# Kernel optimization log

Hardware: AMD Instinct MI355X
Metric: run time of the kernel (lower is better)

The kernel has to match this reference:

```python
import jax, jax.numpy as jnp
import numpy as np

HEADS = 8
DIM_HEAD = 64
DIM = 512
EPS = 1e-5


def setup_inputs() -> dict:
    key = jax.random.key(0)
    ks = jax.random.split(key, 4)
    b, n = 4, 2048
    inner = HEADS * DIM_HEAD
    x = jax.random.normal(ks[0], (b, n, DIM), dtype=jnp.float32)
    pose_bias = jax.random.normal(ks[1], (b, n), dtype=jnp.float32)
    ln_gamma = jnp.ones((DIM,), dtype=jnp.float32)
    ln_beta = jnp.zeros((DIM,), dtype=jnp.float32)
    w_qkv = jax.random.normal(ks[2], (DIM, 3 * inner), dtype=jnp.float32) * (DIM ** -0.5)
    w_out = jax.random.normal(ks[3], (inner, DIM), dtype=jnp.float32) * (inner ** -0.5)
    beta = jnp.float32(0.5)
    return {"x": x, "pose_bias": pose_bias, "ln_gamma": ln_gamma,
            "ln_beta": ln_beta, "w_qkv": w_qkv, "w_out": w_out, "beta": beta}


def reference(x, pose_bias, ln_gamma, ln_beta, w_qkv, w_out, beta):
    b, n, d = x.shape
    h, dh = HEADS, DIM_HEAD
    scale = dh ** -0.5
    # LayerNorm (biased variance, eps=1e-5, affine)
    mu = jnp.mean(x, axis=-1, keepdims=True)
    var = jnp.mean(jnp.square(x - mu), axis=-1, keepdims=True)
    xn = (x - mu) * jax.lax.rsqrt(var + EPS) * ln_gamma + ln_beta
    # fused QKV projection (no bias)
    qkv = xn @ w_qkv                                  # [b, n, 3*h*dh]
    q, k, v = jnp.split(qkv, 3, axis=-1)
    def to_heads(t):
        return t.reshape(b, n, h, dh).transpose(0, 2, 1, 3)  # [b, h, n, dh]
    q, k, v = to_heads(q), to_heads(k), to_heads(v)
    dots = jnp.einsum('bhnd,bhmd->bhnm', q, k) * scale  # [b, h, n, n]
    # additive pose bias: beta * (bias_i + bias_j), broadcast over heads
    pose_attn = beta * (pose_bias[:, None, :, None] + pose_bias[:, None, None, :])
    dots = dots + pose_attn
    attn = jax.nn.softmax(dots, axis=-1)
    out = jnp.einsum('bhnm,bhmd->bhnd', attn, v)       # [b, h, n, dh]
    out = out.transpose(0, 2, 1, 3).reshape(b, n, h * dh)
    return out @ w_out
```

## Files before the change

kernel.cpp:

```cpp
#include <hip/hip_runtime.h>

#define NH    8
#define DH    64
#define DIMD  512
#define NCTX  2048
#define NB    4
#define NROWS (NB * NCTX)
#define QKVN  (3 * DIMD)

typedef __attribute__((ext_vector_type(8))) short bf16x8;
typedef __attribute__((ext_vector_type(4))) float f32x4;

#define INV_LN2 1.44269504f
#define SCLOG   (0.125f * INV_LN2)

__device__ __forceinline__ unsigned short f2bits(float f) {
  unsigned u = __float_as_uint(f);
  u += 0x7fffu + ((u >> 16) & 1u);
  return (unsigned short)(u >> 16);
}
__device__ __forceinline__ float bits2f(unsigned short u) {
  return __uint_as_float(((unsigned)u) << 16);
}

__global__ __launch_bounds__(256) void ln_kernel(
    const float* __restrict__ x,
    const float* __restrict__ gamma,
    const float* __restrict__ beta,
    unsigned short* __restrict__ xn) {
  const int wid  = threadIdx.x >> 6;
  const int lane = threadIdx.x & 63;
  const int row  = blockIdx.x * 4 + wid;
  const float* xr = x + (size_t)row * DIMD + lane * 8;
  float v[8];
  const float4 a = *reinterpret_cast<const float4*>(xr);
  const float4 b = *reinterpret_cast<const float4*>(xr + 4);
  v[0] = a.x; v[1] = a.y; v[2] = a.z; v[3] = a.w;
  v[4] = b.x; v[5] = b.y; v[6] = b.z; v[7] = b.w;
  float s = 0.f;
#pragma unroll
  for (int i = 0; i < 8; ++i) s += v[i];
#pragma unroll
  for (int off = 32; off; off >>= 1) s += __shfl_down(s, off);
  s = __shfl(s, 0);
  const float mu = s * (1.f / DIMD);
  float ss = 0.f;
#pragma unroll
  for (int i = 0; i < 8; ++i) { float d = v[i] - mu; ss += d * d; }
#pragma unroll
  for (int off = 32; off; off >>= 1) ss += __shfl_down(ss, off);
  ss = __shfl(ss, 0);
  const float inv = rsqrtf(ss * (1.f / DIMD) + 1e-5f);
  const float4 g0 = *reinterpret_cast<const float4*>(gamma + lane * 8);
  const float4 g1 = *reinterpret_cast<const float4*>(gamma + lane * 8 + 4);
  const float4 b0 = *reinterpret_cast<const float4*>(beta + lane * 8);
  const float4 b1 = *reinterpret_cast<const float4*>(beta + lane * 8 + 4);
  float g[8] = {g0.x, g0.y, g0.z, g0.w, g1.x, g1.y, g1.z, g1.w};
  float be[8] = {b0.x, b0.y, b0.z, b0.w, b1.x, b1.y, b1.z, b1.w};
  bf16x8 o;
#pragma unroll
  for (int i = 0; i < 8; ++i)
    o[i] = (short)f2bits((v[i] - mu) * inv * g[i] + be[i]);
  *reinterpret_cast<bf16x8*>(xn + (size_t)row * DIMD + lane * 8) = o;
}

__global__ __launch_bounds__(256) void tconv_kernel(
    const float* __restrict__ in0, unsigned short* __restrict__ out0,
    const float* __restrict__ in1, unsigned short* __restrict__ out1) {
  const int z = blockIdx.z;
  const int C = z ? DIMD : QKVN;
  if (z && blockIdx.x >= DIMD / 64) return;
  const float* in = z ? in1 : in0;
  unsigned short* out = z ? out1 : out0;
  __shared__ float T[64][65];
  const int r0 = blockIdx.y * 64, c0 = blockIdx.x * 64;
  const int ty = threadIdx.x >> 4, tx = threadIdx.x & 15;
#pragma unroll
  for (int i = 0; i < 4; ++i) {
    const int r = ty + i * 16;
    const float4 v = *reinterpret_cast<const float4*>(
        in + (size_t)(r0 + r) * C + c0 + tx * 4);
    T[r][tx * 4 + 0] = v.x; T[r][tx * 4 + 1] = v.y;
    T[r][tx * 4 + 2] = v.z; T[r][tx * 4 + 3] = v.w;
  }
  __syncthreads();
#pragma unroll
  for (int i = 0; i < 4; ++i) {
    const int c = ty + i * 16;
    ushort4 o;
    o.x = f2bits(T[tx * 4 + 0][c]); o.y = f2bits(T[tx * 4 + 1][c]);
    o.z = f2bits(T[tx * 4 + 2][c]); o.w = f2bits(T[tx * 4 + 3][c]);
    *reinterpret_cast<ushort4*>(out + (size_t)(c0 + c) * DIMD + r0 + tx * 4) = o;
  }
}

__global__ __launch_bounds__(256) void vtrans_kernel(
    const unsigned short* __restrict__ qkv,
    const float* __restrict__ pb,
    const float* __restrict__ betap,
    unsigned short* __restrict__ cexp,
    unsigned short* __restrict__ vt) {
  __shared__ unsigned short T[64][68];
  const int jt = blockIdx.x, hi = blockIdx.y, bi = blockIdx.z;
  const int ty = threadIdx.x >> 4, tx = threadIdx.x & 15;
  const int j0 = jt * 64;
#pragma unroll
  for (int i = 0; i < 4; ++i) {
    const int j = ty + i * 16;
    const ushort4 v = *reinterpret_cast<const ushort4*>(
        qkv + (size_t)(bi * NCTX + j0 + j) * QKVN + 2 * DIMD + hi * DH + tx * 4);
    T[j][tx * 4 + 0] = v.x; T[j][tx * 4 + 1] = v.y;
    T[j][tx * 4 + 2] = v.z; T[j][tx * 4 + 3] = v.w;
  }
  const float bl2 = betap[0] * INV_LN2;
  const float4 pv = *reinterpret_cast<const float4*>(pb + bi * NCTX + j0 + tx * 4);
  ushort4 cb;
  cb.x = f2bits(exp2f(bl2 * pv.x)); cb.y = f2bits(exp2f(bl2 * pv.y));
  cb.z = f2bits(exp2f(bl2 * pv.z)); cb.w = f2bits(exp2f(bl2 * pv.w));
  if (hi == 0 && ty == 0)
    *reinterpret_cast<ushort4*>(cexp + bi * NCTX + j0 + tx * 4) = cb;
  const float c0 = bits2f(cb.x), c1 = bits2f(cb.y), c2 = bits2f(cb.z), c3 = bits2f(cb.w);
  __syncthreads();
#pragma unroll
  for (int i = 0; i < 4; ++i) {
    const int d = ty + i * 16;
    ushort4 o;
    o.x = f2bits(bits2f(T[tx * 4 + 0][d]) * c0);
    o.y = f2bits(bits2f(T[tx * 4 + 1][d]) * c1);
    o.z = f2bits(bits2f(T[tx * 4 + 2][d]) * c2);
    o.w = f2bits(bits2f(T[tx * 4 + 3][d]) * c3);
    *reinterpret_cast<ushort4*>(
        vt + ((size_t)(bi * NH + hi) * DH + d) * NCTX + j0 + tx * 4) = o;
  }
}

__device__ __forceinline__ void storeC(float* C, size_t idx, float v) { C[idx] = v; }
__device__ __forceinline__ void storeC(unsigned short* C, size_t idx, float v) { C[idx] = f2bits(v); }

template <typename CT, bool QS>
__global__ __launch_bounds__(256) void mgemm_kernel(
    const unsigned short* __restrict__ A, const unsigned short* __restrict__ Bt,
    CT* __restrict__ C, int M, int N, int K) {
  __shared__ __align__(16) unsigned short As[128][72];
  __shared__ __align__(16) unsigned short Bs[128][72];
  const int tid  = threadIdx.x;
  const int wave = tid >> 6, lane = tid & 63;
  const int quad = lane >> 4, l16 = lane & 15;
  const int wr = wave >> 1, wc = wave & 1;
  const int tm0 = blockIdx.y * 128, tn0 = blockIdx.x * 128;
  const int srow = tid >> 3;
  const int schunk = (tid & 7) * 8;
  f32x4 acc[4][4];
#pragma unroll
  for (int i = 0; i < 4; ++i)
#pragma unroll
    for (int j = 0; j < 4; ++j) acc[i][j] = (f32x4){0.f, 0.f, 0.f, 0.f};

  bf16x8 ra[4], rb[4];
#pragma unroll
  for (int p = 0; p < 4; ++p) {
    const int r = srow + p * 32;
    ra[p] = *reinterpret_cast<const bf16x8*>(A + (size_t)(tm0 + r) * K + schunk);
    rb[p] = *reinterpret_cast<const bf16x8*>(Bt + (size_t)(tn0 + r) * K + schunk);
  }
  for (int k0 = 0; k0 < K; k0 += 64) {
#pragma unroll
    for (int p = 0; p < 4; ++p) {
      const int r = srow + p * 32;
      *reinterpret_cast<bf16x8*>(&As[r][schunk]) = ra[p];
      *reinterpret_cast<bf16x8*>(&Bs[r][schunk]) = rb[p];
    }
    __syncthreads();
    if (k0 + 64 < K) {
#pragma unroll
      for (int p = 0; p < 4; ++p) {
        const int r = srow + p * 32;
        ra[p] = *reinterpret_cast<const bf16x8*>(A + (size_t)(tm0 + r) * K + k0 + 64 + schunk);
        rb[p] = *reinterpret_cast<const bf16x8*>(Bt + (size_t)(tn0 + r) * K + k0 + 64 + schunk);
      }
    }
#pragma unroll
    for (int kc = 0; kc < 2; ++kc) {
      const int kk = kc * 32 + quad * 8;
      bf16x8 af[4], bfr[4];
#pragma unroll
      for (int i = 0; i < 4; ++i)
        af[i] = *reinterpret_cast<const bf16x8*>(&As[wr * 64 + i * 16 + l16][kk]);
#pragma unroll
      for (int j = 0; j < 4; ++j)
        bfr[j] = *reinterpret_cast<const bf16x8*>(&Bs[wc * 64 + j * 16 + l16][kk]);
#pragma unroll
      for (int i = 0; i < 4; ++i)
#pragma unroll
        for (int j = 0; j < 4; ++j)
          acc[i][j] = __builtin_amdgcn_mfma_f32_16x16x32_bf16(af[i], bfr[j], acc[i][j], 0, 0, 0);
    }
    __syncthreads();
  }
#pragma unroll
  for (int j = 0; j < 4; ++j) {
    const int col = tn0 + wc * 64 + j * 16 + l16;
    const float scl = (QS && col < DIMD) ? SCLOG : 1.0f;
#pragma unroll
    for (int i = 0; i < 4; ++i)
#pragma unroll
      for (int r = 0; r < 4; ++r)
        storeC(C, (size_t)(tm0 + wr * 64 + i * 16 + quad * 4 + r) * N + col,
               acc[i][j][r] * scl);
  }
}

__global__ __launch_bounds__(256, 4) void fattn_kernel(
    const unsigned short* __restrict__ qkv,
    const unsigned short* __restrict__ vtg,
    const unsigned short* __restrict__ cexp,
    unsigned short* __restrict__ out) {
  __shared__ __align__(16) unsigned short lds[19840];
  unsigned short (*Kl)[72] = (unsigned short (*)[72])(lds + 5120);
  unsigned short (*Vt)[72] = (unsigned short (*)[72])(lds + 9728);
  unsigned short* Ob = lds + 15488;
  float* lb = (float*)(lds + 19584);

  const int qt = blockIdx.x, hi = blockIdx.y, bi = blockIdx.z;
  const int tid  = threadIdx.x;
  const int wave = tid >> 6, lane = tid & 63;
  const int quad = lane >> 4, l16 = lane & 15;
  const int wq = wave & 1, wk = wave >> 1;
  unsigned short* Pw = lds + wave * 1280;
  const int qrow0 = qt * 64;
  const unsigned short* base  = qkv + (size_t)bi * NCTX * QKVN + hi * DH;
  const unsigned short* vbase = vtg + (size_t)(bi * NH + hi) * DH * NCTX;
  const unsigned short* cbase = cexp + (size_t)bi * NCTX;
  const int sr = tid >> 2;
  const int sc4 = (tid & 3) * 16;

  bf16x8 qf[2][2];
#pragma unroll
  for (int u = 0; u < 2; ++u)
#pragma unroll
    for (int h = 0; h < 2; ++h)
      qf[u][h] = *reinterpret_cast<const bf16x8*>(
          base + (size_t)(qrow0 + wq * 32 + u * 16 + l16) * QKVN + h * 32 + quad * 8);
  if (tid < 135) {
    const uint4 z = {0u, 0u, 0u, 0u};
    *reinterpret_cast<uint4*>(&Vt[65 + tid / 9][(tid % 9) * 8]) = z;
  }
  bf16x8 pk0, pk1, pv0, pv1; ushort4 pc;
  {
    const unsigned short* kr = base + (size_t)sr * QKVN + DIMD + sc4;
    pk0 = *reinterpret_cast<const bf16x8*>(kr);
    pk1 = *reinterpret_cast<const bf16x8*>(kr + 8);
    const unsigned short* vr = vbase + (size_t)sr * NCTX + sc4;
    pv0 = *reinterpret_cast<const bf16x8*>(vr);
    pv1 = *reinterpret_cast<const bf16x8*>(vr + 8);
    if (tid < 16) pc = *reinterpret_cast<const ushort4*>(cbase + tid * 4);
    *reinterpret_cast<bf16x8*>(&Kl[sr][sc4])     = pk0;
    *reinterpret_cast<bf16x8*>(&Kl[sr][sc4 + 8]) = pk1;
    *reinterpret_cast<bf16x8*>(&Vt[sr][sc4])     = pv0;
    *reinterpret_cast<bf16x8*>(&Vt[sr][sc4 + 8]) = pv1;
    if (tid < 16) *reinterpret_cast<ushort4*>(&Vt[64][tid * 4]) = pc;
  }
  __syncthreads();

  f32x4 O[2][4], accl[2];
#pragma unroll
  for (int u = 0; u < 2; ++u) {
    accl[u] = (f32x4){0.f, 0.f, 0.f, 0.f};
#pragma unroll
    for (int s = 0; s < 4; ++s) O[u][s] = (f32x4){0.f, 0.f, 0.f, 0.f};
  }

  for (int kt = 0; kt < 32; ++kt) {
    if (kt < 31) {
      const int krow1 = (kt + 1) * 64;
      const unsigned short* kr = base + (size_t)(krow1 + sr) * QKVN + DIMD + sc4;
      pk0 = *reinterpret_cast<const bf16x8*>(kr);
      pk1 = *reinterpret_cast<const bf16x8*>(kr + 8);
      const unsigned short* vr = vbase + (size_t)sr * NCTX + krow1 + sc4;
      pv0 = *reinterpret_cast<const bf16x8*>(vr);
      pv1 = *reinterpret_cast<const bf16x8*>(vr + 8);
      if (tid < 16) pc = *reinterpret_cast<const ushort4*>(cbase + krow1 + tid * 4);
    }
    f32x4 sfr[2][2];
#pragma unroll
    for (int t = 0; t < 2; ++t) {
      const bf16x8 kf0 = *reinterpret_cast<const bf16x8*>(
          &Kl[wk * 32 + t * 16 + l16][quad * 8]);
      const bf16x8 kf1 = *reinterpret_cast<const bf16x8*>(
          &Kl[wk * 32 + t * 16 + l16][32 + quad * 8]);
#pragma unroll
      for (int u = 0; u < 2; ++u) {
        f32x4 acc = (f32x4){0.f, 0.f, 0.f, 0.f};
        acc = __builtin_amdgcn_mfma_f32_16x16x32_bf16(kf0, qf[u][0], acc, 0, 0, 0);
        acc = __builtin_amdgcn_mfma_f32_16x16x32_bf16(kf1, qf[u][1], acc, 0, 0, 0);
        sfr[t][u] = acc;
      }
    }
#pragma unroll
    for (int t = 0; t < 2; ++t)
#pragma unroll
      for (int u = 0; u < 2; ++u) {
        const unsigned u0 = __float_as_uint(exp2f(sfr[t][u][0])) + 0x8000u;
        const unsigned u1 = __float_as_uint(exp2f(sfr[t][u][1])) + 0x8000u;
        const unsigned u2 = __float_as_uint(exp2f(sfr[t][u][2])) + 0x8000u;
        const unsigned u3 = __float_as_uint(exp2f(sfr[t][u][3])) + 0x8000u;
        uint2 pw;
        pw.x = __builtin_amdgcn_perm(u1, u0, 0x07060302u);
        pw.y = __builtin_amdgcn_perm(u3, u2, 0x07060302u);
        *reinterpret_cast<uint2*>(&Pw[(u * 16 + l16) * 40 + t * 16 + quad * 4]) = pw;
      }
    {
      const bf16x8 cf = *reinterpret_cast<const bf16x8*>(
          &Vt[64 + l16][wk * 32 + quad * 8]);
#pragma unroll
      for (int u = 0; u < 2; ++u) {
        const bf16x8 pf = *reinterpret_cast<const bf16x8*>(
            &Pw[(u * 16 + l16) * 40 + quad * 8]);
#pragma unroll
        for (int s = 0; s < 4; ++s) {
          const bf16x8 bv = *reinterpret_cast<const bf16x8*>(
              &Vt[s * 16 + l16][wk * 32 + quad * 8]);
          O[u][s] = __builtin_amdgcn_mfma_f32_16x16x32_bf16(pf, bv, O[u][s], 0, 0, 0);
        }
        accl[u] = __builtin_amdgcn_mfma_f32_16x16x32_bf16(pf, cf, accl[u], 0, 0, 0);
      }
    }
    if (kt < 31) {
      __syncthreads();
      *reinterpret_cast<bf16x8*>(&Kl[sr][sc4])     = pk0;
      *reinterpret_cast<bf16x8*>(&Kl[sr][sc4 + 8]) = pk1;
      *reinterpret_cast<bf16x8*>(&Vt[sr][sc4])     = pv0;
      *reinterpret_cast<bf16x8*>(&Vt[sr][sc4 + 8]) = pv1;
      if (tid < 16) *reinterpret_cast<ushort4*>(&Vt[64][tid * 4]) = pc;
      __syncthreads();
    }
  }
  __syncthreads();
  if (wk == 1) {
#pragma unroll
    for (int u = 0; u < 2; ++u) {
#pragma unroll
      for (int s = 0; s < 4; ++s)
#pragma unroll
        for (int r = 0; r < 4; ++r)
          Ob[(wq * 32 + u * 16 + quad * 4 + r) * 64 + s * 16 + l16] = f2bits(O[u][s][r]);
      if (l16 == 0)
#pragma unroll
        for (int r = 0; r < 4; ++r)
          lb[64 + wq * 32 + u * 16 + quad * 4 + r] = accl[u][r];
    }
  } else {
#pragma unroll
    for (int u = 0; u < 2; ++u)
      if (l16 == 0)
#pragma unroll
        for (int r = 0; r < 4; ++r)
          lb[wq * 32 + u * 16 + quad * 4 + r] = accl[u][r];
  }
  __syncthreads();
  if (wk == 0) {
#pragma unroll
    for (int u = 0; u < 2; ++u)
#pragma unroll
      for (int r = 0; r < 4; ++r) {
        const int ql = wq * 32 + u * 16 + quad * 4 + r;
        const float linv = 1.f / (lb[ql] + lb[64 + ql]);
        const size_t orow = ((size_t)bi * NCTX + qrow0 + ql) * DIMD + hi * DH;
#pragma unroll
        for (int s = 0; s < 4; ++s)
          out[orow + s * 16 + l16] =
              f2bits((O[u][s][r] + bits2f(Ob[ql * 64 + s * 16 + l16])) * linv);
      }
  }
}

extern "C" void kernel_launch(void* const* d_in, const int* in_sizes, int n_in,
                              void* d_out, int out_size, void* d_ws, size_t ws_size,
                              hipStream_t stream) {
  const float* x     = (const float*)d_in[0];
  const float* pose  = (const float*)d_in[1];
  const float* gam   = (const float*)d_in[2];
  const float* bet   = (const float*)d_in[3];
  const float* wqkv  = (const float*)d_in[4];
  const float* wout  = (const float*)d_in[5];
  const float* betap = (const float*)d_in[6];
  float* out = (float*)d_out;

  unsigned short* xn    = (unsigned short*)d_ws;
  unsigned short* qkvb  = xn + (size_t)NROWS * DIMD;
  unsigned short* wqkvT = qkvb + (size_t)NROWS * QKVN;
  unsigned short* woutT = wqkvT + (size_t)QKVN * DIMD;
  unsigned short* vtg   = woutT + (size_t)DIMD * DIMD;
  unsigned short* cexp  = vtg + (size_t)NB * NH * DH * NCTX;
  unsigned short* aout  = xn;

  ln_kernel<<<NROWS / 4, 256, 0, stream>>>(x, gam, bet, xn);
  tconv_kernel<<<dim3(QKVN / 64, DIMD / 64, 2), 256, 0, stream>>>(
      wqkv, wqkvT, wout, woutT);
  mgemm_kernel<unsigned short, true><<<dim3(QKVN / 128, NROWS / 128), 256, 0, stream>>>(
      xn, wqkvT, qkvb, NROWS, QKVN, DIMD);
  vtrans_kernel<<<dim3(NCTX / 64, NH, NB), 256, 0, stream>>>(
      qkvb, pose, betap, cexp, vtg);
  fattn_kernel<<<dim3(NCTX / 64, NH, NB), 256, 0, stream>>>(qkvb, vtg, cexp, aout);
  mgemm_kernel<float, false><<<dim3(DIMD / 128, NROWS / 128), 256, 0, stream>>>(
      aout, woutT, out, NROWS, DIMD, DIMD);
}
```

Baseline: 178.4 us.

## Keep softmax probabilities in registers via permlane swaps instead of LDS round-trip

The exp'd score tile is now packed to bf16 with v_cvt_pk_bf16_f32 and rearranged into the MFMA A-operand layout using v_permlane32/16_swap, rather than being written to a per-wave LDS buffer and read back. This drops the P staging area, shrinks LDS from about 39KB to about 18.5KB (which could raise occupancy), moves the rowsum c-row to a small separate buffer, and pads the output reduction buffer stride to 68. It also switches from truncation-with-rounding bias to a hardware conversion. It depends on the permlane swap lane mapping being correct and on gfx950-specific instructions.

```diff
diff --git a/kernel.cpp b/kernel.cpp
--- a/kernel.cpp
+++ b/kernel.cpp
@@ -215,18 +215,18 @@
     const unsigned short* __restrict__ vtg,
     const unsigned short* __restrict__ cexp,
     unsigned short* __restrict__ out) {
-  __shared__ __align__(16) unsigned short lds[19840];
-  unsigned short (*Kl)[72] = (unsigned short (*)[72])(lds + 5120);
-  unsigned short (*Vt)[72] = (unsigned short (*)[72])(lds + 9728);
-  unsigned short* Ob = lds + 15488;
-  float* lb = (float*)(lds + 19584);
+  __shared__ __align__(16) unsigned short lds[9280];
+  unsigned short (*Kl)[72] = (unsigned short (*)[72])(lds);
+  unsigned short (*Vt)[72] = (unsigned short (*)[72])(lds + 4608);
+  unsigned short* crow = lds + 9216;
+  unsigned short* Ob = lds;
+  float* lb = (float*)(lds + 4352);
 
   const int qt = blockIdx.x, hi = blockIdx.y, bi = blockIdx.z;
   const int tid  = threadIdx.x;
   const int wave = tid >> 6, lane = tid & 63;
   const int quad = lane >> 4, l16 = lane & 15;
   const int wq = wave & 1, wk = wave >> 1;
-  unsigned short* Pw = lds + wave * 1280;
   const int qrow0 = qt * 64;
   const unsigned short* base  = qkv + (size_t)bi * NCTX * QKVN + hi * DH;
   const unsigned short* vbase = vtg + (size_t)(bi * NH + hi) * DH * NCTX;
@@ -241,10 +241,6 @@
     for (int h = 0; h < 2; ++h)
       qf[u][h] = *reinterpret_cast<const bf16x8*>(
           base + (size_t)(qrow0 + wq * 32 + u * 16 + l16) * QKVN + h * 32 + quad * 8);
-  if (tid < 135) {
-    const uint4 z = {0u, 0u, 0u, 0u};
-    *reinterpret_cast<uint4*>(&Vt[65 + tid / 9][(tid % 9) * 8]) = z;
-  }
   bf16x8 pk0, pk1, pv0, pv1; ushort4 pc;
   {
     const unsigned short* kr = base + (size_t)sr * QKVN + DIMD + sc4;
@@ -258,7 +254,7 @@
     *reinterpret_cast<bf16x8*>(&Kl[sr][sc4 + 8]) = pk1;
     *reinterpret_cast<bf16x8*>(&Vt[sr][sc4])     = pv0;
     *reinterpret_cast<bf16x8*>(&Vt[sr][sc4 + 8]) = pv1;
-    if (tid < 16) *reinterpret_cast<ushort4*>(&Vt[64][tid * 4]) = pc;
+    if (tid < 16) *reinterpret_cast<ushort4*>(&crow[tid * 4]) = pc;
   }
   __syncthreads();
 
@@ -296,33 +292,38 @@
         sfr[t][u] = acc;
       }
     }
-#pragma unroll
-    for (int t = 0; t < 2; ++t)
-#pragma unroll
-      for (int u = 0; u < 2; ++u) {
-        const unsigned u0 = __float_as_uint(exp2f(sfr[t][u][0])) + 0x8000u;
-        const unsigned u1 = __float_as_uint(exp2f(sfr[t][u][1])) + 0x8000u;
-        const unsigned u2 = __float_as_uint(exp2f(sfr[t][u][2])) + 0x8000u;
-        const unsigned u3 = __float_as_uint(exp2f(sfr[t][u][3])) + 0x8000u;
-        uint2 pw;
-        pw.x = __builtin_amdgcn_perm(u1, u0, 0x07060302u);
-        pw.y = __builtin_amdgcn_perm(u3, u2, 0x07060302u);
-        *reinterpret_cast<uint2*>(&Pw[(u * 16 + l16) * 40 + t * 16 + quad * 4]) = pw;
+    bf16x8 pf[2];
+#pragma unroll
+    for (int u = 0; u < 2; ++u) {
+      unsigned x0, x1, y0, y1;
+      {
+        const float e0 = exp2f(sfr[0][u][0]), e1 = exp2f(sfr[0][u][1]);
+        const float e2 = exp2f(sfr[0][u][2]), e3 = exp2f(sfr[0][u][3]);
+        const float f0 = exp2f(sfr[1][u][0]), f1 = exp2f(sfr[1][u][1]);
+        const float f2 = exp2f(sfr[1][u][2]), f3 = exp2f(sfr[1][u][3]);
+        asm("v_cvt_pk_bf16_f32 %0, %1, %2" : "=v"(x0) : "v"(e0), "v"(e1));
+        asm("v_cvt_pk_bf16_f32 %0, %1, %2" : "=v"(x1) : "v"(e2), "v"(e3));
+        asm("v_cvt_pk_bf16_f32 %0, %1, %2" : "=v"(y0) : "v"(f0), "v"(f1));
+        asm("v_cvt_pk_bf16_f32 %0, %1, %2" : "=v"(y1) : "v"(f2), "v"(f3));
       }
+      asm("v_permlane32_swap_b32 %0, %1" : "+v"(x0), "+v"(y0));
+      asm("v_permlane32_swap_b32 %0, %1" : "+v"(x1), "+v"(y1));
+      asm("v_permlane16_swap_b32 %0, %1" : "+v"(x0), "+v"(y0));
+      asm("v_permlane16_swap_b32 %0, %1" : "+v"(x1), "+v"(y1));
+      union { unsigned q[4]; bf16x8 v; } pu;
+      pu.q[0] = x0; pu.q[1] = x1; pu.q[2] = y0; pu.q[3] = y1;
+      pf[u] = pu.v;
+    }
     {
-      const bf16x8 cf = *reinterpret_cast<const bf16x8*>(
-          &Vt[64 + l16][wk * 32 + quad * 8]);
-#pragma unroll
-      for (int u = 0; u < 2; ++u) {
-        const bf16x8 pf = *reinterpret_cast<const bf16x8*>(
-            &Pw[(u * 16 + l16) * 40 + quad * 8]);
-#pragma unroll
-        for (int s = 0; s < 4; ++s) {
-          const bf16x8 bv = *reinterpret_cast<const bf16x8*>(
-              &Vt[s * 16 + l16][wk * 32 + quad * 8]);
-          O[u][s] = __builtin_amdgcn_mfma_f32_16x16x32_bf16(pf, bv, O[u][s], 0, 0, 0);
-        }
-        accl[u] = __builtin_amdgcn_mfma_f32_16x16x32_bf16(pf, cf, accl[u], 0, 0, 0);
+      const bf16x8 cf = *reinterpret_cast<const bf16x8*>(&crow[wk * 32 + quad * 8]);
+      accl[0] = __builtin_amdgcn_mfma_f32_16x16x32_bf16(pf[0], cf, accl[0], 0, 0, 0);
+      accl[1] = __builtin_amdgcn_mfma_f32_16x16x32_bf16(pf[1], cf, accl[1], 0, 0, 0);
+#pragma unroll
+      for (int s = 0; s < 4; ++s) {
+        const bf16x8 bv = *reinterpret_cast<const bf16x8*>(
+            &Vt[s * 16 + l16][wk * 32 + quad * 8]);
+        O[0][s] = __builtin_amdgcn_mfma_f32_16x16x32_bf16(pf[0], bv, O[0][s], 0, 0, 0);
+        O[1][s] = __builtin_amdgcn_mfma_f32_16x16x32_bf16(pf[1], bv, O[1][s], 0, 0, 0);
       }
     }
     if (kt < 31) {
@@ -331,7 +332,7 @@
       *reinterpret_cast<bf16x8*>(&Kl[sr][sc4 + 8]) = pk1;
       *reinterpret_cast<bf16x8*>(&Vt[sr][sc4])     = pv0;
       *reinterpret_cast<bf16x8*>(&Vt[sr][sc4 + 8]) = pv1;
-      if (tid < 16) *reinterpret_cast<ushort4*>(&Vt[64][tid * 4]) = pc;
+      if (tid < 16) *reinterpret_cast<ushort4*>(&crow[tid * 4]) = pc;
       __syncthreads();
     }
   }
@@ -343,7 +344,7 @@
       for (int s = 0; s < 4; ++s)
 #pragma unroll
         for (int r = 0; r < 4; ++r)
-          Ob[(wq * 32 + u * 16 + quad * 4 + r) * 64 + s * 16 + l16] = f2bits(O[u][s][r]);
+          Ob[(wq * 32 + u * 16 + quad * 4 + r) * 68 + s * 16 + l16] = f2bits(O[u][s][r]);
       if (l16 == 0)
 #pragma unroll
         for (int r = 0; r < 4; ++r)
@@ -369,7 +370,7 @@
 #pragma unroll
         for (int s = 0; s < 4; ++s)
           out[orow + s * 16 + l16] =
-              f2bits((O[u][s][r] + bits2f(Ob[ql * 64 + s * 16 + l16])) * linv);
+              f2bits((O[u][s][r] + bits2f(Ob[ql * 68 + s * 16 + l16])) * linv);
       }
   }
 }
```

Measured after the change: 178.3 us. Within noise of the previous version (-0.0%).
